# Kernel optimization log

Hardware: AMD Instinct MI355X
Metric: run time of the kernel (lower is better)

## Reference

```python
import jax, jax.numpy as jnp
import numpy as np

B, T_ENC, U = 8, 200, 100
VOCAB, ENC_DIM, PRED_DIM, EMBED_DIM = 1024, 512, 512, 128


def setup_inputs() -> dict:
    key = jax.random.key(0)
    ks = jax.random.split(key, 13)
    n = lambda k, shape, fan_in: (jax.random.normal(k, shape, jnp.float32) / np.sqrt(fan_in)).astype(jnp.float32)
    return {
        "enc_out": jax.random.normal(ks[0], (B, T_ENC, ENC_DIM), jnp.float32),
        "targets": jax.random.randint(ks[1], (B, U), 0, VOCAB, jnp.int32),
        "target_len": jnp.full((B,), U, jnp.int32),
        # params
        "emb_table": n(ks[2], (VOCAB + 1, EMBED_DIM), 1.0),
        "W_ih": n(ks[3], (4 * PRED_DIM, EMBED_DIM), EMBED_DIM),
        "W_hh": n(ks[4], (4 * PRED_DIM, PRED_DIM), PRED_DIM),
        "b_ih": jnp.zeros((4 * PRED_DIM,), jnp.float32),
        "b_hh": jnp.zeros((4 * PRED_DIM,), jnp.float32),
        "W_enc": n(ks[5], (PRED_DIM, ENC_DIM), ENC_DIM),
        "b_enc": jnp.zeros((PRED_DIM,), jnp.float32),
        "W_pred": n(ks[6], (PRED_DIM, PRED_DIM), PRED_DIM),
        "b_pred": jnp.zeros((PRED_DIM,), jnp.float32),
        "W_joint": n(ks[7], (VOCAB + 1, PRED_DIM), PRED_DIM),
        "b_joint": jnp.zeros((VOCAB + 1,), jnp.float32),
    }


def reference(enc_out, targets, target_len, emb_table, W_ih, W_hh, b_ih, b_hh,
              W_enc, b_enc, W_pred, b_pred, W_joint, b_joint):
    # targets_with_blank: prepend blank_id = vocab_size
    blank_id = emb_table.shape[0] - 1
    Bsz = targets.shape[0]
    tw = jnp.concatenate([jnp.full((Bsz, 1), blank_id, targets.dtype), targets], axis=1)
    emb = emb_table[tw]  # (B, U+1, E)

    P = W_hh.shape[1]
    h0 = jnp.zeros((Bsz, P), emb.dtype)

    def lstm_step(carry, x_t):
        h, c = carry
        gates = x_t @ W_ih.T + b_ih + h @ W_hh.T + b_hh  # (B, 4P)
        i, f, g, o = jnp.split(gates, 4, axis=-1)  # PyTorch LSTMCell gate order
        i, f, o = jax.nn.sigmoid(i), jax.nn.sigmoid(f), jax.nn.sigmoid(o)
        c = f * c + i * jnp.tanh(g)
        h = o * jnp.tanh(c)
        return (h, c), h

    _, pred = jax.lax.scan(lstm_step, (h0, h0), jnp.swapaxes(emb, 0, 1))
    pred = jnp.swapaxes(pred, 0, 1)  # (B, U+1, P)

    f_enc = enc_out @ W_enc.T + b_enc   # (B, T, P)
    f_pred = pred @ W_pred.T + b_pred   # (B, U+1, P)
    joint = jnp.tanh(f_enc[:, :, None, :] + f_pred[:, None, :, :])  # (B, T, U+1, P)
    logits = joint @ W_joint.T + b_joint  # (B, T, U+1, V+1)
    return logits
```

## Files before the change

kernel.cpp:

```cpp
#include <hip/hip_runtime.h>
#include <stdint.h>
#include <stddef.h>

#define BB 8
#define TENC 200
#define UU 100
#define UP1 101
#define VP1 1025
#define ED 128
#define PD 512
#define LSTM_NWG 64

typedef __attribute__((ext_vector_type(8))) unsigned short ushort8;
typedef __attribute__((ext_vector_type(8))) __bf16 bf16x8;
typedef __attribute__((ext_vector_type(4))) float f32x4;

__device__ __forceinline__ float bf2f(unsigned short u){
  unsigned int x = ((unsigned int)u) << 16;
  return __builtin_bit_cast(float, x);
}
__device__ __forceinline__ unsigned short f2bf(float f){
  unsigned int x = __builtin_bit_cast(unsigned int, f);
  unsigned int r = (x + 0x7fffu + ((x >> 16) & 1u)) >> 16;
  return (unsigned short)r;
}
__device__ __forceinline__ float tanh_fast(float x){
  float e = __expf(2.0f * x);
  return 1.0f - 2.0f / (e + 1.0f);
}
__device__ __forceinline__ float sigm(float x){
  return 1.0f / (1.0f + __expf(-x));
}
__device__ __forceinline__ void gload_lds16(const unsigned short* gsrc, unsigned short* ldst){
  __builtin_amdgcn_global_load_lds((const __attribute__((address_space(1))) void*)gsrc,
                                   (__attribute__((address_space(3))) void*)ldst, 16, 0, 0);
}

__global__ __launch_bounds__(256) void k_cvt_bf16(const float* __restrict__ src,
                                                  unsigned short* __restrict__ dst, int n){
  int i = blockIdx.x * 256 + threadIdx.x;
  if (i < n) dst[i] = f2bf(src[i]);
}

__global__ __launch_bounds__(256) void k_xgate(
    const float* __restrict__ emb, const int* __restrict__ targets,
    const float* __restrict__ W_ih, const float* __restrict__ b_ih,
    const float* __restrict__ b_hh, float* __restrict__ xg)
{
  __shared__ float e_s[BB * ED];
  const int u  = blockIdx.x >> 2;
  const int jq = blockIdx.x & 3;
  const int tid = threadIdx.x;
  for (int idx = tid; idx < BB * ED; idx += 256){
    int b = idx >> 7, e = idx & 127;
    int tok = (u == 0) ? 1024 : targets[b * UU + (u - 1)];
    e_s[idx] = emb[(size_t)tok * ED + e];
  }
  __syncthreads();
  float acc[2][BB];
  #pragma unroll
  for (int r = 0; r < 2; r++)
    #pragma unroll
    for (int b = 0; b < BB; b++) acc[r][b] = 0.0f;
  const int j0 = jq * 512 + tid;
  const float* w0p = W_ih + (size_t)j0 * ED;
  const float* w1p = W_ih + (size_t)(j0 + 256) * ED;
  for (int e = 0; e < ED; e++){
    float w0 = w0p[e], w1 = w1p[e];
    #pragma unroll
    for (int b = 0; b < BB; b++){
      float ev = e_s[b * ED + e];
      acc[0][b] = fmaf(ev, w0, acc[0][b]);
      acc[1][b] = fmaf(ev, w1, acc[1][b]);
    }
  }
  #pragma unroll
  for (int r = 0; r < 2; r++){
    int j = j0 + r * 256;
    float bias = b_ih[j] + b_hh[j];
    #pragma unroll
    for (int b = 0; b < BB; b++)
      xg[((size_t)b * UP1 + u) * 2048 + j] = acc[r][b] + bias;
  }
}

__global__ __launch_bounds__(256) void k_lstm_all(
    const float* __restrict__ xg, const float* __restrict__ W_hh,
    float* __restrict__ pred, unsigned int* __restrict__ cnt)
{
  __shared__ float h_s[8][520];
  __shared__ float red[32 * 257];
  __shared__ float gates_s[32][9];
  const int tid = threadIdx.x;
  const int wg  = blockIdx.x;
  const int p0  = wg * 8;
  const int jg = tid >> 5, kc = tid & 31;
  const float* wrow[4];
  #pragma unroll
  for (int r = 0; r < 4; r++){
    int jl = jg * 4 + r;
    int grow = (jl >> 3) * PD + p0 + (jl & 7);
    wrow[r] = W_hh + (size_t)grow * PD;
  }
  float c_reg = 0.0f;
  for (int u = 0; u < UP1; u++){
    float xi = 0.f, xf = 0.f, xgv = 0.f, xo = 0.f;
    if (tid < 64){
      int pl = tid >> 3, b = tid & 7;
      const float* xr = xg + ((size_t)(b * UP1 + u)) * 2048;
      int p = p0 + pl;
      xi = xr[p]; xf = xr[512 + p]; xgv = xr[1024 + p]; xo = xr[1536 + p];
    }
    if (u > 0){
      if (tid == 0){
        while (__hip_atomic_load(&cnt[u - 1], __ATOMIC_RELAXED, __HIP_MEMORY_SCOPE_AGENT) < LSTM_NWG)
          __builtin_amdgcn_s_sleep(8);
      }
      __syncthreads();
      float tmp[16];
      #pragma unroll
      for (int j = 0; j < 16; j++){
        int i = tid + 256 * j;
        int b2 = i >> 9, k = i & 511;
        tmp[j] = __hip_atomic_load(pred + ((size_t)(b2 * UP1 + (u - 1))) * PD + k,
                                   __ATOMIC_RELAXED, __HIP_MEMORY_SCOPE_AGENT);
      }
      #pragma unroll
      for (int j = 0; j < 16; j++){
        int i = tid + 256 * j;
        h_s[i >> 9][i & 511] = tmp[j];
      }
    } else {
      for (int i = tid; i < 8 * PD; i += 256) h_s[i >> 9][i & 511] = 0.0f;
    }
    __syncthreads();
    float acc[4][BB];
    #pragma unroll
    for (int r = 0; r < 4; r++)
      #pragma unroll
      for (int b = 0; b < BB; b++) acc[r][b] = 0.0f;
    for (int i = 0; i < 16; i++){
      int k = kc + 32 * i;
      float hv[BB];
      #pragma unroll
      for (int b = 0; b < BB; b++) hv[b] = h_s[b][k];
      #pragma unroll
      for (int r = 0; r < 4; r++){
        float wv = wrow[r][k];
        #pragma unroll
        for (int b = 0; b < BB; b++) acc[r][b] = fmaf(hv[b], wv, acc[r][b]);
      }
    }
    #pragma unroll
    for (int r = 0; r < 4; r++)
      #pragma unroll
      for (int b = 0; b < BB; b++)
        red[kc * 257 + jg * 32 + r * 8 + b] = acc[r][b];
    __syncthreads();
    {
      int jl = tid >> 3, b = tid & 7;
      float s = 0.0f;
      #pragma unroll
      for (int kk = 0; kk < 32; kk++)
        s += red[kk * 257 + (jl >> 2) * 32 + (jl & 3) * 8 + b];
      gates_s[jl][b] = s;
    }
    __syncthreads();
    if (tid < 64){
      int pl = tid >> 3, b = tid & 7;
      int p = p0 + pl;
      float gi = gates_s[0  + pl][b] + xi;
      float gf = gates_s[8  + pl][b] + xf;
      float gg = gates_s[16 + pl][b] + xgv;
      float go = gates_s[24 + pl][b] + xo;
      float iv = sigm(gi), fv = sigm(gf), ov = sigm(go);
      c_reg = fv * c_reg + iv * tanh_fast(gg);
      float hval = ov * tanh_fast(c_reg);
      __hip_atomic_store(pred + ((size_t)(b * UP1 + u)) * PD + p, hval,
                         __ATOMIC_RELAXED, __HIP_MEMORY_SCOPE_AGENT);
    }
    if (u < UP1 - 1){
      if (tid == 0){
        asm volatile("s_waitcnt vmcnt(0)" ::: "memory");
        __hip_atomic_fetch_add(&cnt[u], 1u, __ATOMIC_RELAXED, __HIP_MEMORY_SCOPE_AGENT);
      }
    }
  }
}

__global__ __launch_bounds__(256) void k_gemm_bias_bf16(
    const float* __restrict__ A, const float* __restrict__ W,
    const float* __restrict__ bias, unsigned short* __restrict__ out, int M)
{
  __shared__ float a_s[16][68];
  __shared__ float b_s[16][68];
  const int m0 = blockIdx.x * 64, n0 = blockIdx.y * 64;
  const int tid = threadIdx.x;
  const int tx = tid & 15, ty = tid >> 4;
  float acc[4][4];
  #pragma unroll
  for (int i2 = 0; i2 < 4; i2++)
    #pragma unroll
    for (int j2 = 0; j2 < 4; j2++) acc[i2][j2] = 0.0f;
  for (int k0 = 0; k0 < 512; k0 += 16){
    int mm = tid >> 2, k4 = (tid & 3) * 4;
    int row = m0 + mm; if (row >= M) row = M - 1;
    float4 av = *(const float4*)(A + (size_t)row * 512 + k0 + k4);
    a_s[k4 + 0][mm] = av.x; a_s[k4 + 1][mm] = av.y;
    a_s[k4 + 2][mm] = av.z; a_s[k4 + 3][mm] = av.w;
    float4 bv = *(const float4*)(W + (size_t)(n0 + mm) * 512 + k0 + k4);
    b_s[k4 + 0][mm] = bv.x; b_s[k4 + 1][mm] = bv.y;
    b_s[k4 + 2][mm] = bv.z; b_s[k4 + 3][mm] = bv.w;
    __syncthreads();
    #pragma unroll
    for (int k = 0; k < 16; k++){
      float4 a4 = *(const float4*)&a_s[k][ty * 4];
      float4 b4 = *(const float4*)&b_s[k][tx * 4];
      float aa[4] = {a4.x, a4.y, a4.z, a4.w};
      float bb[4] = {b4.x, b4.y, b4.z, b4.w};
      #pragma unroll
      for (int i2 = 0; i2 < 4; i2++)
        #pragma unroll
        for (int j2 = 0; j2 < 4; j2++)
          acc[i2][j2] = fmaf(aa[i2], bb[j2], acc[i2][j2]);
    }
    __syncthreads();
  }
  #pragma unroll
  for (int i2 = 0; i2 < 4; i2++){
    int m = m0 + ty * 4 + i2;
    if (m < M){
      #pragma unroll
      for (int j2 = 0; j2 < 4; j2++){
        int n = n0 + tx * 4 + j2;
        out[(size_t)m * 512 + n] = f2bf(acc[i2][j2] + bias[n]);
      }
    }
  }
}

__global__ __launch_bounds__(512, 1) void k_joint3(
    const unsigned short* __restrict__ fe, const unsigned short* __restrict__ fp,
    const unsigned short* __restrict__ wj, const float* __restrict__ bj,
    float* __restrict__ out)
{
  __shared__ unsigned short A_s[128 * 512];
  __shared__ unsigned short B_s[3][128 * 32];
  const int tu = blockIdx.x;
  const int b  = blockIdx.y;
  const int tt = tu / 13, ut = tu - tt * 13;
  const int t0 = tt * 16, u0 = ut * 8;
  const int tid = threadIdx.x;
  const int w = tid >> 6, l = tid & 63;
  const int l15 = l & 15, lg = l >> 4;
  const int wr = w >> 1, wc = w & 1;

  auto issue = [&](int idx){
    int nt = idx >> 4, ks = idx & 15;
    int rb = tid >> 2, cs = tid & 3;
    int col8 = cs ^ ((rb >> 1) & 3);
    const unsigned short* src = wj + (size_t)(nt * 128 + rb) * 512 + ks * 32 + col8 * 8;
    gload_lds16(src, (unsigned short*)B_s[idx % 3] + (size_t)(w * 64) * 8);
  };

  issue(0);

  for (int rr = 0; rr < 16; rr++){
    int row = rr * 8 + w;
    int ti = row >> 3, ui = row & 7;
    int t = t0 + ti, uu = u0 + ui;
    ushort8 a = {0,0,0,0,0,0,0,0};
    if (t < TENC && uu < UP1){
      ushort8 f8 = *(const ushort8*)(fe + (size_t)(b * TENC + t) * 512 + l * 8);
      ushort8 p8 = *(const ushort8*)(fp + (size_t)(b * UP1 + uu) * 512 + l * 8);
      #pragma unroll
      for (int j = 0; j < 8; j++)
        a[j] = f2bf(tanh_fast(bf2f(f8[j]) + bf2f(p8[j])));
    }
    int byteo = row * 1024 + ((l * 16) ^ ((row & 7) << 4));
    *(ushort8*)((char*)A_s + byteo) = a;
  }
  __syncthreads();

  f32x4 acc[2][4];
  #pragma unroll
  for (int fr = 0; fr < 2; fr++)
    #pragma unroll
    for (int fc = 0; fc < 4; fc++)
      acc[fr][fc] = (f32x4){0.f, 0.f, 0.f, 0.f};

  for (int idx = 0; idx < 128; idx++){
    const int nt = idx >> 4, ks = idx & 15;
    if (idx + 1 < 128){
      issue(idx + 1);
      asm volatile("s_waitcnt vmcnt(1)" ::: "memory");
    } else {
      asm volatile("s_waitcnt vmcnt(0)" ::: "memory");
    }
    __builtin_amdgcn_s_barrier();

    const unsigned short* bb = (const unsigned short*)B_s[idx % 3];
    bf16x8 bfr[4], afr[2];
    #pragma unroll
    for (int fc = 0; fc < 4; fc++){
      int rb = wc * 64 + fc * 16 + l15;
      int byteo = rb * 64 + ((lg ^ ((rb >> 1) & 3)) * 16);
      bfr[fc] = __builtin_bit_cast(bf16x8, *(const ushort8*)((const char*)bb + byteo));
    }
    #pragma unroll
    for (int fr = 0; fr < 2; fr++){
      int ra = wr * 32 + fr * 16 + l15;
      int k8 = ks * 4 + lg;
      int byteo = ra * 1024 + ((k8 * 16) ^ ((ra & 7) << 4));
      afr[fr] = __builtin_bit_cast(bf16x8, *(const ushort8*)((const char*)A_s + byteo));
    }
    #pragma unroll
    for (int fr = 0; fr < 2; fr++)
      #pragma unroll
      for (int fc = 0; fc < 4; fc++)
        acc[fr][fc] = __builtin_amdgcn_mfma_f32_16x16x32_bf16(bfr[fc], afr[fr], acc[fr][fc], 0, 0, 0);

    if (ks == 15){
      #pragma unroll
      for (int fr = 0; fr < 2; fr++){
        int m = wr * 32 + fr * 16 + l15;
        int t = t0 + (m >> 3), uu2 = u0 + (m & 7);
        if (t < TENC && uu2 < UP1){
          float* orow = out + ((size_t)(b * TENC + t) * UP1 + uu2) * VP1;
          #pragma unroll
          for (int fc = 0; fc < 4; fc++){
            int nb = nt * 128 + wc * 64 + fc * 16 + lg * 4;
            float4 bv = *(const float4*)(bj + nb);
            f32x4 v = acc[fr][fc];
            float4 st = {v[0] + bv.x, v[1] + bv.y, v[2] + bv.z, v[3] + bv.w};
            *(float4*)(orow + nb) = st;
          }
        }
        #pragma unroll
        for (int fc = 0; fc < 4; fc++)
          acc[fr][fc] = (f32x4){0.f, 0.f, 0.f, 0.f};
      }
    }
  }

  {
    int row = tid >> 2, q = tid & 3;
    float s = 0.0f;
    const unsigned short* w1 = wj + (size_t)1024 * 512;
    #pragma unroll 4
    for (int j = 0; j < 16; j++){
      int k8 = q * 16 + j;
      int byteo = row * 1024 + ((k8 * 16) ^ ((row & 7) << 4));
      ushort8 a8 = *(const ushort8*)((const char*)A_s + byteo);
      ushort8 w8 = *(const ushort8*)(w1 + k8 * 8);
      #pragma unroll
      for (int jj = 0; jj < 8; jj++)
        s += bf2f(a8[jj]) * bf2f(w8[jj]);
    }
    s += __shfl_xor(s, 1);
    s += __shfl_xor(s, 2);
    if (q == 0){
      int t = t0 + (row >> 3), uu = u0 + (row & 7);
      if (t < TENC && uu < UP1)
        out[((size_t)(b * TENC + t) * UP1 + uu) * VP1 + 1024] = s + bj[1024];
    }
  }
}

extern "C" void kernel_launch(void* const* d_in, const int* in_sizes, int n_in,
                              void* d_out, int out_size, void* d_ws, size_t ws_size,
                              hipStream_t stream) {
  const float* enc_out = (const float*)d_in[0];
  const int*   targets = (const int*)d_in[1];
  const float* emb     = (const float*)d_in[3];
  const float* W_ih    = (const float*)d_in[4];
  const float* W_hh    = (const float*)d_in[5];
  const float* b_ih    = (const float*)d_in[6];
  const float* b_hh    = (const float*)d_in[7];
  const float* W_enc   = (const float*)d_in[8];
  const float* b_enc   = (const float*)d_in[9];
  const float* W_pred  = (const float*)d_in[10];
  const float* b_pred  = (const float*)d_in[11];
  const float* W_joint = (const float*)d_in[12];
  const float* b_joint = (const float*)d_in[13];
  float* out = (float*)d_out;

  char* ws = (char*)d_ws;
  float* xg            = (float*)(ws + 0);
  float* pred          = (float*)(ws + 6619136);
  unsigned short* feb  = (unsigned short*)(ws + 8273920);
  unsigned short* fpb  = (unsigned short*)(ws + 9912320);
  unsigned short* wjb  = (unsigned short*)(ws + 10739712);
  unsigned int*   cnt  = (unsigned int*)(ws + 11789312);

  hipMemsetAsync(cnt, 0, UP1 * sizeof(unsigned int), stream);
  hipLaunchKernelGGL(k_cvt_bf16, dim3((VP1 * 512 + 255) / 256), dim3(256), 0, stream,
                     W_joint, wjb, VP1 * 512);
  hipLaunchKernelGGL(k_xgate, dim3(404), dim3(256), 0, stream,
                     emb, targets, W_ih, b_ih, b_hh, xg);
  hipLaunchKernelGGL(k_gemm_bias_bf16, dim3(25, 8), dim3(256), 0, stream,
                     enc_out, W_enc, b_enc, feb, 1600);
  hipLaunchKernelGGL(k_lstm_all, dim3(LSTM_NWG), dim3(256), 0, stream,
                     xg, W_hh, pred, cnt);
  hipLaunchKernelGGL(k_gemm_bias_bf16, dim3(13, 8), dim3(256), 0, stream,
                     pred, W_pred, b_pred, fpb, 808);
  hipLaunchKernelGGL(k_joint3, dim3(169, 8), dim3(512), 0, stream,
                     feb, fpb, wjb, b_joint, out);
}
```

Measured before the change: 1.004 ms.

## Retile joint GEMM as flat M×N tiles, split blank column, double-buffer LSTM h

The joint kernel is restructured from per-(t,u)-block tiles that loop over all vocab tiles into a flat 2D grid of 128x128 output tiles over all B*T*(U+1) rows. Each tile recomputes tanh(f_enc+f_pred) for its A slice and double-buffers A and B through registers into LDS, with two 256-thread blocks allowed per CU. The blank column becomes a separate scalar kernel. The LSTM now exchanges h through a small contiguous ping-pong buffer with a shorter spin sleep. The cost is recomputing tanh once per vocab tile (8x) and losing the async global-to-LDS loads.

New measurement: 1.122 ms. +11.7%, slower.

```diff
diff --git a/kernel.cpp b/kernel.cpp
--- a/kernel.cpp
+++ b/kernel.cpp
@@ -10,6 +10,7 @@
 #define ED 128
 #define PD 512
 #define LSTM_NWG 64
+#define MTOT 161600
 
 typedef __attribute__((ext_vector_type(8))) unsigned short ushort8;
 typedef __attribute__((ext_vector_type(8))) __bf16 bf16x8;
@@ -30,10 +31,6 @@
 }
 __device__ __forceinline__ float sigm(float x){
   return 1.0f / (1.0f + __expf(-x));
-}
-__device__ __forceinline__ void gload_lds16(const unsigned short* gsrc, unsigned short* ldst){
-  __builtin_amdgcn_global_load_lds((const __attribute__((address_space(1))) void*)gsrc,
-                                   (__attribute__((address_space(3))) void*)ldst, 16, 0, 0);
 }
 
 __global__ __launch_bounds__(256) void k_cvt_bf16(const float* __restrict__ src,
@@ -86,7 +83,7 @@
 
 __global__ __launch_bounds__(256) void k_lstm_all(
     const float* __restrict__ xg, const float* __restrict__ W_hh,
-    float* __restrict__ pred, unsigned int* __restrict__ cnt)
+    float* __restrict__ pred, float* __restrict__ hb, unsigned int* __restrict__ cnt)
 {
   __shared__ float h_s[8][520];
   __shared__ float red[32 * 257];
@@ -114,17 +111,15 @@
     if (u > 0){
       if (tid == 0){
         while (__hip_atomic_load(&cnt[u - 1], __ATOMIC_RELAXED, __HIP_MEMORY_SCOPE_AGENT) < LSTM_NWG)
-          __builtin_amdgcn_s_sleep(8);
+          __builtin_amdgcn_s_sleep(2);
       }
       __syncthreads();
+      const float* hsrc = hb + ((u - 1) & 1) * 4096;
       float tmp[16];
       #pragma unroll
-      for (int j = 0; j < 16; j++){
-        int i = tid + 256 * j;
-        int b2 = i >> 9, k = i & 511;
-        tmp[j] = __hip_atomic_load(pred + ((size_t)(b2 * UP1 + (u - 1))) * PD + k,
+      for (int j = 0; j < 16; j++)
+        tmp[j] = __hip_atomic_load(hsrc + tid + 256 * j,
                                    __ATOMIC_RELAXED, __HIP_MEMORY_SCOPE_AGENT);
-      }
       #pragma unroll
       for (int j = 0; j < 16; j++){
         int i = tid + 256 * j;
@@ -167,23 +162,22 @@
     }
     __syncthreads();
     if (tid < 64){
-      int pl = tid >> 3, b = tid & 7;
+      int pl = tid >> 3, b2 = tid & 7;
       int p = p0 + pl;
-      float gi = gates_s[0  + pl][b] + xi;
-      float gf = gates_s[8  + pl][b] + xf;
-      float gg = gates_s[16 + pl][b] + xgv;
-      float go = gates_s[24 + pl][b] + xo;
+      float gi = gates_s[0  + pl][b2] + xi;
+      float gf = gates_s[8  + pl][b2] + xf;
+      float gg = gates_s[16 + pl][b2] + xgv;
+      float go = gates_s[24 + pl][b2] + xo;
       float iv = sigm(gi), fv = sigm(gf), ov = sigm(go);
       c_reg = fv * c_reg + iv * tanh_fast(gg);
       float hval = ov * tanh_fast(c_reg);
-      __hip_atomic_store(pred + ((size_t)(b * UP1 + u)) * PD + p, hval,
+      __hip_atomic_store(hb + (u & 1) * 4096 + b2 * 512 + p, hval,
                          __ATOMIC_RELAXED, __HIP_MEMORY_SCOPE_AGENT);
-    }
-    if (u < UP1 - 1){
-      if (tid == 0){
-        asm volatile("s_waitcnt vmcnt(0)" ::: "memory");
-        __hip_atomic_fetch_add(&cnt[u], 1u, __ATOMIC_RELAXED, __HIP_MEMORY_SCOPE_AGENT);
-      }
+      pred[((size_t)(b2 * UP1 + u)) * PD + p] = hval;
+    }
+    if (u < UP1 - 1 && tid == 0){
+      asm volatile("s_waitcnt vmcnt(0)" ::: "memory");
+      __hip_atomic_fetch_add(&cnt[u], 1u, __ATOMIC_RELAXED, __HIP_MEMORY_SCOPE_AGENT);
     }
   }
 }
@@ -239,132 +233,133 @@
   }
 }
 
-__global__ __launch_bounds__(512, 1) void k_joint3(
+__global__ __launch_bounds__(256, 2) void k_joint6(
     const unsigned short* __restrict__ fe, const unsigned short* __restrict__ fp,
     const unsigned short* __restrict__ wj, const float* __restrict__ bj,
     float* __restrict__ out)
 {
-  __shared__ unsigned short A_s[128 * 512];
-  __shared__ unsigned short B_s[3][128 * 32];
-  const int tu = blockIdx.x;
-  const int b  = blockIdx.y;
-  const int tt = tu / 13, ut = tu - tt * 13;
-  const int t0 = tt * 16, u0 = ut * 8;
+  __shared__ unsigned short A_s[2][128 * 64];
+  __shared__ unsigned short B_s[2][128 * 64];
+  const int m0 = blockIdx.x * 128;
+  const int n0 = blockIdx.y * 128;
   const int tid = threadIdx.x;
   const int w = tid >> 6, l = tid & 63;
   const int l15 = l & 15, lg = l >> 4;
   const int wr = w >> 1, wc = w & 1;
 
-  auto issue = [&](int idx){
-    int nt = idx >> 4, ks = idx & 15;
-    int rb = tid >> 2, cs = tid & 3;
-    int col8 = cs ^ ((rb >> 1) & 3);
-    const unsigned short* src = wj + (size_t)(nt * 128 + rb) * 512 + ks * 32 + col8 * 8;
-    gload_lds16(src, (unsigned short*)B_s[idx % 3] + (size_t)(w * 64) * 8);
+  const int sr = tid >> 1;
+  const int sh = (tid & 1) * 32;
+  int mclamp = m0 + sr; if (mclamp >= MTOT) mclamp = MTOT - 1;
+  const int q  = mclamp / 101;
+  const int su = mclamp - q * 101;
+  const int sb = q / 200;
+  const unsigned short* fe_row = fe + (size_t)q * 512 + sh;
+  const unsigned short* fp_row = fp + (size_t)(sb * 101 + su) * 512 + sh;
+  const unsigned short* wj_row = wj + (size_t)(n0 + sr) * 512 + sh;
+
+  ushort8 rfe[4], rfp[4], rwj[4];
+  auto load_regs = [&](int kc0){
+    #pragma unroll
+    for (int j = 0; j < 4; j++){
+      rfe[j] = *(const ushort8*)(fe_row + kc0 + j * 8);
+      rfp[j] = *(const ushort8*)(fp_row + kc0 + j * 8);
+      rwj[j] = *(const ushort8*)(wj_row + kc0 + j * 8);
+    }
   };
-
-  issue(0);
-
-  for (int rr = 0; rr < 16; rr++){
-    int row = rr * 8 + w;
-    int ti = row >> 3, ui = row & 7;
-    int t = t0 + ti, uu = u0 + ui;
-    ushort8 a = {0,0,0,0,0,0,0,0};
-    if (t < TENC && uu < UP1){
-      ushort8 f8 = *(const ushort8*)(fe + (size_t)(b * TENC + t) * 512 + l * 8);
-      ushort8 p8 = *(const ushort8*)(fp + (size_t)(b * UP1 + uu) * 512 + l * 8);
-      #pragma unroll
-      for (int j = 0; j < 8; j++)
-        a[j] = f2bf(tanh_fast(bf2f(f8[j]) + bf2f(p8[j])));
-    }
-    int byteo = row * 1024 + ((l * 16) ^ ((row & 7) << 4));
-    *(ushort8*)((char*)A_s + byteo) = a;
-  }
+  auto write_lds = [&](int buf){
+    #pragma unroll
+    for (int j = 0; j < 4; j++){
+      ushort8 a;
+      #pragma unroll
+      for (int e = 0; e < 8; e++)
+        a[e] = f2bf(tanh_fast(bf2f(rfe[j][e]) + bf2f(rfp[j][e])));
+      int byo = sr * 128 + (((sh + j * 8) * 2) ^ ((sr & 7) << 4));
+      *(ushort8*)((char*)A_s[buf] + byo) = a;
+      *(ushort8*)((char*)B_s[buf] + byo) = rwj[j];
+    }
+  };
+
+  load_regs(0);
+  write_lds(0);
   __syncthreads();
 
-  f32x4 acc[2][4];
-  #pragma unroll
-  for (int fr = 0; fr < 2; fr++)
+  f32x4 acc[4][4];
+  #pragma unroll
+  for (int fr = 0; fr < 4; fr++)
     #pragma unroll
     for (int fc = 0; fc < 4; fc++)
       acc[fr][fc] = (f32x4){0.f, 0.f, 0.f, 0.f};
 
-  for (int idx = 0; idx < 128; idx++){
-    const int nt = idx >> 4, ks = idx & 15;
-    if (idx + 1 < 128){
-      issue(idx + 1);
-      asm volatile("s_waitcnt vmcnt(1)" ::: "memory");
-    } else {
-      asm volatile("s_waitcnt vmcnt(0)" ::: "memory");
-    }
-    __builtin_amdgcn_s_barrier();
-
-    const unsigned short* bb = (const unsigned short*)B_s[idx % 3];
-    bf16x8 bfr[4], afr[2];
-    #pragma unroll
-    for (int fc = 0; fc < 4; fc++){
-      int rb = wc * 64 + fc * 16 + l15;
-      int byteo = rb * 64 + ((lg ^ ((rb >> 1) & 3)) * 16);
-      bfr[fc] = __builtin_bit_cast(bf16x8, *(const ushort8*)((const char*)bb + byteo));
-    }
-    #pragma unroll
-    for (int fr = 0; fr < 2; fr++){
-      int ra = wr * 32 + fr * 16 + l15;
-      int k8 = ks * 4 + lg;
-      int byteo = ra * 1024 + ((k8 * 16) ^ ((ra & 7) << 4));
-      afr[fr] = __builtin_bit_cast(bf16x8, *(const ushort8*)((const char*)A_s + byteo));
-    }
-    #pragma unroll
-    for (int fr = 0; fr < 2; fr++)
-      #pragma unroll
-      for (int fc = 0; fc < 4; fc++)
-        acc[fr][fc] = __builtin_amdgcn_mfma_f32_16x16x32_bf16(bfr[fc], afr[fr], acc[fr][fc], 0, 0, 0);
-
-    if (ks == 15){
-      #pragma unroll
-      for (int fr = 0; fr < 2; fr++){
-        int m = wr * 32 + fr * 16 + l15;
-        int t = t0 + (m >> 3), uu2 = u0 + (m & 7);
-        if (t < TENC && uu2 < UP1){
-          float* orow = out + ((size_t)(b * TENC + t) * UP1 + uu2) * VP1;
-          #pragma unroll
-          for (int fc = 0; fc < 4; fc++){
-            int nb = nt * 128 + wc * 64 + fc * 16 + lg * 4;
-            float4 bv = *(const float4*)(bj + nb);
-            f32x4 v = acc[fr][fc];
-            float4 st = {v[0] + bv.x, v[1] + bv.y, v[2] + bv.z, v[3] + bv.w};
-            *(float4*)(orow + nb) = st;
-          }
-        }
+  for (int kc = 0; kc < 8; kc++){
+    const int buf = kc & 1;
+    if (kc < 7) load_regs((kc + 1) * 64);
+    #pragma unroll
+    for (int ks = 0; ks < 2; ks++){
+      bf16x8 afr[4], bfr[4];
+      #pragma unroll
+      for (int f = 0; f < 4; f++){
+        int ra = wr * 64 + f * 16 + l15;
+        int bya = ra * 128 + ((ks * 64 + lg * 16) ^ ((ra & 7) << 4));
+        afr[f] = __builtin_bit_cast(bf16x8, *(const ushort8*)((const char*)A_s[buf] + bya));
+        int rb = wc * 64 + f * 16 + l15;
+        int byb = rb * 128 + ((ks * 64 + lg * 16) ^ ((rb & 7) << 4));
+        bfr[f] = __builtin_bit_cast(bf16x8, *(const ushort8*)((const char*)B_s[buf] + byb));
+      }
+      #pragma unroll
+      for (int fr = 0; fr < 4; fr++)
         #pragma unroll
         for (int fc = 0; fc < 4; fc++)
-          acc[fr][fc] = (f32x4){0.f, 0.f, 0.f, 0.f};
-      }
-    }
-  }
-
-  {
-    int row = tid >> 2, q = tid & 3;
-    float s = 0.0f;
-    const unsigned short* w1 = wj + (size_t)1024 * 512;
-    #pragma unroll 4
-    for (int j = 0; j < 16; j++){
-      int k8 = q * 16 + j;
-      int byteo = row * 1024 + ((k8 * 16) ^ ((row & 7) << 4));
-      ushort8 a8 = *(const ushort8*)((const char*)A_s + byteo);
-      ushort8 w8 = *(const ushort8*)(w1 + k8 * 8);
-      #pragma unroll
-      for (int jj = 0; jj < 8; jj++)
-        s += bf2f(a8[jj]) * bf2f(w8[jj]);
-    }
-    s += __shfl_xor(s, 1);
-    s += __shfl_xor(s, 2);
-    if (q == 0){
-      int t = t0 + (row >> 3), uu = u0 + (row & 7);
-      if (t < TENC && uu < UP1)
-        out[((size_t)(b * TENC + t) * UP1 + uu) * VP1 + 1024] = s + bj[1024];
-    }
-  }
+          acc[fr][fc] = __builtin_amdgcn_mfma_f32_16x16x32_bf16(bfr[fc], afr[fr], acc[fr][fc], 0, 0, 0);
+    }
+    if (kc < 7) write_lds(buf ^ 1);
+    __syncthreads();
+  }
+
+  #pragma unroll
+  for (int fr = 0; fr < 4; fr++){
+    int m = m0 + wr * 64 + fr * 16 + l15;
+    if (m < MTOT){
+      float* orow = out + (size_t)m * VP1;
+      #pragma unroll
+      for (int fc = 0; fc < 4; fc++){
+        int col = n0 + wc * 64 + fc * 16 + lg * 4;
+        float4 bv = *(const float4*)(bj + col);
+        f32x4 v = acc[fr][fc];
+        float4 st = {v[0] + bv.x, v[1] + bv.y, v[2] + bv.z, v[3] + bv.w};
+        *(float4*)(orow + col) = st;
+      }
+    }
+  }
+}
+
+__global__ __launch_bounds__(256) void k_blank(
+    const unsigned short* __restrict__ fe, const unsigned short* __restrict__ fp,
+    const unsigned short* __restrict__ wj, const float* __restrict__ bj,
+    float* __restrict__ out)
+{
+  __shared__ float w_s[512];
+  const int tid = threadIdx.x;
+  const unsigned short* w1 = wj + (size_t)1024 * 512;
+  w_s[tid]       = bf2f(w1[tid]);
+  w_s[tid + 256] = bf2f(w1[tid + 256]);
+  __syncthreads();
+  int m = blockIdx.x * 256 + tid;
+  if (m >= MTOT) return;
+  const int q  = m / 101;
+  const int u  = m - q * 101;
+  const int b  = q / 200;
+  const unsigned short* fe_row = fe + (size_t)q * 512;
+  const unsigned short* fp_row = fp + (size_t)(b * 101 + u) * 512;
+  float s = 0.0f;
+  #pragma unroll 4
+  for (int k = 0; k < 512; k += 8){
+    ushort8 f8 = *(const ushort8*)(fe_row + k);
+    ushort8 p8 = *(const ushort8*)(fp_row + k);
+    #pragma unroll
+    for (int e = 0; e < 8; e++)
+      s += tanh_fast(bf2f(f8[e]) + bf2f(p8[e])) * w_s[k + e];
+  }
+  out[(size_t)m * VP1 + 1024] = s + bj[1024];
 }
 
 extern "C" void kernel_launch(void* const* d_in, const int* in_sizes, int n_in,
@@ -391,9 +386,10 @@
   unsigned short* feb  = (unsigned short*)(ws + 8273920);
   unsigned short* fpb  = (unsigned short*)(ws + 9912320);
   unsigned short* wjb  = (unsigned short*)(ws + 10739712);
-  unsigned int*   cnt  = (unsigned int*)(ws + 11789312);
-
-  hipMemsetAsync(cnt, 0, UP1 * sizeof(unsigned int), stream);
+  float* hb            = (float*)(ws + 11789312);
+  unsigned int* cnt    = (unsigned int*)(ws + 11822080);
+
+  (void)hipMemsetAsync(cnt, 0, UP1 * sizeof(unsigned int), stream);
   hipLaunchKernelGGL(k_cvt_bf16, dim3((VP1 * 512 + 255) / 256), dim3(256), 0, stream,
                      W_joint, wjb, VP1 * 512);
   hipLaunchKernelGGL(k_xgate, dim3(404), dim3(256), 0, stream,
@@ -401,9 +397,11 @@
   hipLaunchKernelGGL(k_gemm_bias_bf16, dim3(25, 8), dim3(256), 0, stream,
                      enc_out, W_enc, b_enc, feb, 1600);
   hipLaunchKernelGGL(k_lstm_all, dim3(LSTM_NWG), dim3(256), 0, stream,
-                     xg, W_hh, pred, cnt);
+                     xg, W_hh, pred, hb, cnt);
   hipLaunchKernelGGL(k_gemm_bias_bf16, dim3(13, 8), dim3(256), 0, stream,
                      pred, W_pred, b_pred, fpb, 808);
-  hipLaunchKernelGGL(k_joint3, dim3(169, 8), dim3(512), 0, stream,
+  hipLaunchKernelGGL(k_joint6, dim3(1263, 8), dim3(256), 0, stream,
                      feb, fpb, wjb, b_joint, out);
-}
+  hipLaunchKernelGGL(k_blank, dim3((MTOT + 255) / 256), dim3(256), 0, stream,
+                     feb, fpb, wjb, b_joint, out);
+}
```
